# Kernel optimization log

Hardware: AMD Instinct MI355X
Metric: run time of the kernel (lower is better)

Reference implementation:

```python
import jax, jax.numpy as jnp
import numpy as np

NG, ND, CIN = 100000, 50000, 128
H, D = 8, 32
HID = H * D
E = 200000
SCALE = 1.0 / np.sqrt(D)


def _segment_softmax(logits, seg, num):
    # logits: [E, H]; softmax over edges sharing the same destination node
    m = jax.ops.segment_max(logits, seg, num_segments=num)
    m = jnp.where(jnp.isfinite(m), m, 0.0)  # guard empty segments
    e = jnp.exp(logits - m[seg])
    s = jax.ops.segment_sum(e, seg, num_segments=num)
    return e / (s[seg] + 1e-16)


def _kqv(x, Wk, bk, Wq, bq, Wv, bv):
    n = x.shape[0]
    return ((x @ Wk + bk).reshape(n, H, D),
            (x @ Wq + bq).reshape(n, H, D),
            (x @ Wv + bv).reshape(n, H, D))


def _message(k_src, v_src, q_dst, src, dst, a_rel, m_rel, p_rel, n_dst):
    # per-edge-type relation transform of gathered K/V, softmax over dst, scatter-add
    k_e = jnp.einsum('ehd,hdf->ehf', k_src[src], a_rel)          # [E,H,D]
    v_e = jnp.einsum('ehd,hdf->ehf', v_src[src], m_rel)          # [E,H,D]
    logits = jnp.einsum('ehf,ehf->eh', q_dst[dst], k_e) * p_rel * SCALE
    alpha = _segment_softmax(logits, dst, n_dst)                 # [E,H]
    return jax.ops.segment_sum(alpha[..., None] * v_e, dst, num_segments=n_dst)


def _forward(x_gene, x_disease, Win_g, bin_g, Wk_g, bk_g, Wq_g, bq_g, Wv_g, bv_g,
             Wa_g, ba_g, skip_g, Win_d, bin_d, Wk_d, bk_d, Wq_d, bq_d, Wv_d, bv_d,
             Wa_d, ba_d, skip_d, a_g2d, m_g2d, p_g2d, a_d2g, m_d2g, p_d2g,
             a_g2g, m_g2g, p_g2g, prelu_w,
             g2d_src, g2d_dst, d2g_src, d2g_dst, g2g_src, g2g_dst):
    # per-type input projection (Encoder.lin_dict)
    xg = x_gene @ Win_g + bin_g      # [NG, HID]
    xd = x_disease @ Win_d + bin_d   # [ND, HID]
    ng, nd = xg.shape[0], xd.shape[0]
    kg, qg, vg = _kqv(xg, Wk_g, bk_g, Wq_g, bq_g, Wv_g, bv_g)
    kd, qd, vd = _kqv(xd, Wk_d, bk_d, Wq_d, bq_d, Wv_d, bv_d)
    # HGTConv: message passing per edge type, summed per destination type
    out_d = _message(kg, vg, qd, g2d_src, g2d_dst, a_g2d, m_g2d, p_g2d, nd)
    out_g = (_message(kd, vd, qg, d2g_src, d2g_dst, a_d2g, m_d2g, p_d2g, ng)
             + _message(kg, vg, qg, g2g_src, g2g_dst, a_g2g, m_g2g, p_g2g, ng))

    def finish(out, x_proj, Wa, ba, skip):
        h = jax.nn.gelu(out.reshape(-1, HID), approximate=False) @ Wa + ba
        beta = jax.nn.sigmoid(skip)
        h = beta * h + (1.0 - beta) * x_proj          # HGT skip connection
        return jnp.where(h > 0, h, prelu_w * h)       # PReLU; Dropout=identity (eval)

    return (finish(out_g, xg, Wa_g, ba_g, skip_g),
            finish(out_d, xd, Wa_d, ba_d, skip_d))


def setup_inputs():
    key = jax.random.key(0)
    ki = iter(jax.random.split(key, 64))
    def nrm(shape, s):
        return (jax.random.normal(next(ki), shape) * s).astype(jnp.float32)
    inp = {}
    inp['x_gene'] = jax.random.normal(next(ki), (NG, CIN), jnp.float32)
    inp['x_disease'] = jax.random.normal(next(ki), (ND, CIN), jnp.float32)
    for t in ('g', 'd'):
        inp[f'Win_{t}'] = nrm((CIN, HID), 0.09)
        inp[f'bin_{t}'] = jnp.zeros((HID,), jnp.float32)
        for p in ('k', 'q', 'v'):
            inp[f'W{p}_{t}'] = nrm((HID, HID), 0.06)
            inp[f'b{p}_{t}'] = jnp.zeros((HID,), jnp.float32)
        inp[f'Wa_{t}'] = nrm((HID, HID), 0.06)
        inp[f'ba_{t}'] = jnp.zeros((HID,), jnp.float32)
        inp[f'skip_{t}'] = jnp.ones((1,), jnp.float32)
    for r in ('g2d', 'd2g', 'g2g'):
        inp[f'a_{r}'] = nrm((H, D, D), 0.18)
        inp[f'm_{r}'] = nrm((H, D, D), 0.18)
        inp[f'p_{r}'] = jnp.ones((H,), jnp.float32)
    inp['prelu_w'] = jnp.full((HID,), 0.25, jnp.float32)
    sizes = {'g2d': (NG, ND), 'd2g': (ND, NG), 'g2g': (NG, NG)}
    for r, (ns_, nd_) in sizes.items():
        inp[f'{r}_src'] = jax.random.randint(next(ki), (E,), 0, ns_, jnp.int32)
        inp[f'{r}_dst'] = jax.random.randint(next(ki), (E,), 0, nd_, jnp.int32)
    return inp


def reference(x_gene, x_disease, Win_g, bin_g, Wk_g, bk_g, Wq_g, bq_g, Wv_g, bv_g,
              Wa_g, ba_g, skip_g, Win_d, bin_d, Wk_d, bk_d, Wq_d, bq_d, Wv_d, bv_d,
              Wa_d, ba_d, skip_d, a_g2d, m_g2d, p_g2d, a_d2g, m_d2g, p_d2g,
              a_g2g, m_g2g, p_g2g, prelu_w,
              g2d_src, g2d_dst, d2g_src, d2g_dst, g2g_src, g2g_dst):
    return _forward(x_gene, x_disease, Win_g, bin_g, Wk_g, bk_g, Wq_g, bq_g, Wv_g, bv_g,
                    Wa_g, ba_g, skip_g, Win_d, bin_d, Wk_d, bk_d, Wq_d, bq_d, Wv_d, bv_d,
                    Wa_d, ba_d, skip_d, a_g2d, m_g2d, p_g2d, a_d2g, m_d2g, p_d2g,
                    a_g2g, m_g2g, p_g2g, prelu_w,
                    g2d_src, g2d_dst, d2g_src, d2g_dst, g2g_src, g2g_dst)
```

## Files before the change

kernel.cpp:

```cpp
#include <hip/hip_runtime.h>
#include <hip/hip_bf16.h>
#include <math.h>

typedef unsigned short u16;
typedef __attribute__((ext_vector_type(4))) float f32x4;
typedef __attribute__((ext_vector_type(8))) short s16x8;

__device__ __forceinline__ float b2f(u16 u){
  union { unsigned u; float f; } v; v.u = ((unsigned)u) << 16; return v.f;
}
__device__ __forceinline__ u16 f2b(float f){
  union { float f; unsigned u; } v; v.f = f;
  unsigned r = v.u + 0x7fffu + ((v.u >> 16) & 1u);
  return (u16)(r >> 16);
}

__device__ __forceinline__ void gload_lds(const u16* g, u16* l){
  __builtin_amdgcn_global_load_lds(
      (const __attribute__((address_space(1))) unsigned*)g,
      (__attribute__((address_space(3))) unsigned*)l, 16, 0, 0);
}

__global__ void zero_k(int* __restrict__ p, int n){
  int i = blockIdx.x*256 + threadIdx.x;
  if(i < n) p[i] = 0;
}

struct T6 { const float* W[6]; u16* O[6]; int K[6]; };
__global__ void transpose6(T6 a){
  int r = blockIdx.y;
  int idx = blockIdx.x*256 + threadIdx.x;
  int K = a.K[r];
  if(idx < K*256){ int k = idx >> 8, n = idx & 255; a.O[r][n*K + k] = f2b(a.W[r][idx]); }
}

struct F6 { const float* Wk[6]; const float* A[6]; u16* O[6]; };
__global__ void foldw6(F6 fa){
  int r = blockIdx.y;
  int idx = blockIdx.x*256 + threadIdx.x;
  int n = idx >> 8, k = idx & 255;
  int h = n >> 5, f = n & 31;
  const float* Wk = fa.Wk[r]; const float* A = fa.A[r];
  float s = 0.f;
  #pragma unroll 8
  for(int d = 0; d < 32; d++)
    s += Wk[k*256 + h*32 + d] * A[h*1024 + d*32 + f];
  fa.O[r][n*256 + k] = f2b(s);
}

struct Fb6 { const float* bk[6]; const float* A[6]; float* O[6]; };
__global__ void foldb6(Fb6 fa){
  int r = blockIdx.x;
  int n = threadIdx.x;
  int h = n >> 5, f = n & 31;
  float s = 0.f;
  for(int d = 0; d < 32; d++)
    s += fa.bk[r][h*32 + d] * fa.A[r][h*1024 + d*32 + f];
  fa.O[r][n] = s;
}

struct CSR3 {
  const int* src[3]; const int* dst[3]; int n[3];
  int* cnt[3]; int* rs[3]; int* cur[3]; int* col[3]; int* tot[3];
};
__global__ void count3(CSR3 c, int E){
  int r = blockIdx.y;
  int e = blockIdx.x*256 + threadIdx.x;
  if(e < E) atomicAdd(&c.cnt[r][c.dst[r][e]], 1);
}
__global__ void alloc3(CSR3 c){
  int r = blockIdx.y;
  int i = blockIdx.x*256 + threadIdx.x;
  if(i < c.n[r]) c.rs[r][i] = atomicAdd(c.tot[r], c.cnt[r][i]);
}
__global__ void fill3(CSR3 c, int E){
  int r = blockIdx.y;
  int e = blockIdx.x*256 + threadIdx.x;
  if(e < E){
    int d = c.dst[r][e];
    int p = c.rs[r][d] + atomicAdd(&c.cur[r][d], 1);
    c.col[r][p] = c.src[r][e];
  }
}

template<int AF, int EPI>
__global__ __launch_bounds__(256) void gemm128(
    const void* __restrict__ Ap, const u16* __restrict__ BT,
    const float* __restrict__ bias, void* __restrict__ Cout,
    int M, int K, int lda, int ldc,
    const u16* __restrict__ X, const float* __restrict__ skip,
    const float* __restrict__ prelu)
{
  constexpr int BM = (EPI == 2) ? 64 : 128;
  constexpr int BN = (EPI == 2) ? 256 : 128;
  __shared__ u16 As[BM*32];
  __shared__ u16 Bs[BN*32];
  const int t = threadIdx.x;
  const int m0 = blockIdx.x * BM;
  const int n0 = blockIdx.y * BN;
  const int w = t >> 6, lane = t & 63;
  const int wm = (EPI==2) ? 0 : ((w >> 1) << 6);
  const int wn = (EPI==2) ? (w << 6) : ((w & 1) << 6);
  const int lr = lane & 15, lq = lane >> 4;
  const int jr = lane >> 2;
  const int sp = lane & 3;
  f32x4 acc[4][4];
  #pragma unroll
  for(int i=0;i<4;i++)
    #pragma unroll
    for(int j=0;j<4;j++) acc[i][j] = (f32x4){0.f,0.f,0.f,0.f};

  for(int k0 = 0; k0 < K; k0 += 32){
    if(AF){
      const float* Af = (const float*)Ap;
      constexpr int NS = BM*4;
      #pragma unroll
      for(int j = 0; j < NS/256; j++){
        int s = t + j*256;
        int rr = s >> 2, p2 = s & 3;
        int sl = p2 ^ (rr & 3);
        int gm = m0 + rr; if(gm > M-1) gm = M-1;
        const float* g = Af + (size_t)gm*lda + k0 + sl*8;
        float4 f0 = *(const float4*)g;
        float4 f1 = *(const float4*)(g + 4);
        s16x8 v;
        v[0]=(short)f2b(f0.x); v[1]=(short)f2b(f0.y); v[2]=(short)f2b(f0.z); v[3]=(short)f2b(f0.w);
        v[4]=(short)f2b(f1.x); v[5]=(short)f2b(f1.y); v[6]=(short)f2b(f1.z); v[7]=(short)f2b(f1.w);
        *(s16x8*)&As[rr*32 + p2*8] = v;
      }
    } else {
      const u16* Ab = (const u16*)Ap;
      constexpr int RA = BM/4;
      #pragma unroll
      for(int i = 0; i < RA/16; i++){
        int rr = w*RA + i*16 + jr;
        int sl = sp ^ (rr & 3);
        int gm = m0 + rr; if(gm > M-1) gm = M-1;
        gload_lds(Ab + (size_t)gm*lda + k0 + sl*8, &As[(w*RA + i*16)*32]);
      }
    }
    {
      constexpr int RB = BN/4;
      #pragma unroll
      for(int i = 0; i < RB/16; i++){
        int rr = w*RB + i*16 + jr;
        int sl = sp ^ (rr & 3);
        gload_lds(BT + (size_t)(n0 + rr)*K + k0 + sl*8, &Bs[(w*RB + i*16)*32]);
      }
    }
    __syncthreads();
    s16x8 a[4], b[4];
    #pragma unroll
    for(int mt=0; mt<4; mt++)
      a[mt] = *(const s16x8*)&As[(wm + mt*16 + lr)*32 + ((lq ^ (lr&3)) << 3)];
    #pragma unroll
    for(int nt=0; nt<4; nt++)
      b[nt] = *(const s16x8*)&Bs[(wn + nt*16 + lr)*32 + ((lq ^ (lr&3)) << 3)];
    #pragma unroll
    for(int mt=0; mt<4; mt++)
      #pragma unroll
      for(int nt=0; nt<4; nt++)
        acc[mt][nt] = __builtin_amdgcn_mfma_f32_16x16x32_bf16(a[mt], b[nt], acc[mt][nt], 0, 0, 0);
    __syncthreads();
  }

  float beta = 0.f;
  if(EPI == 2) beta = 1.f/(1.f + __expf(-skip[0]));
  #pragma unroll
  for(int nt=0; nt<4; nt++){
    const int col = n0 + wn + nt*16 + lr;
    const float bcol = bias[col];
    float pw = 0.f;
    if(EPI == 2) pw = prelu[col];
    #pragma unroll
    for(int mt=0; mt<4; mt++){
      #pragma unroll
      for(int i=0;i<4;i++){
        int row = m0 + wm + mt*16 + lq*4 + i;
        if(row < M){
          float v = acc[mt][nt][i] + bcol;
          if(EPI == 0) ((u16*)Cout)[(size_t)row*ldc + col] = f2b(v);
          else if(EPI == 1) ((float*)Cout)[(size_t)row*ldc + col] = v;
          else {
            float xv = b2f(X[(size_t)row*256 + col]);
            v = beta*v + (1.f - beta)*xv;
            v = v > 0.f ? v : pw*v;
            ((float*)Cout)[(size_t)row*ldc + col] = v;
          }
        }
      }
    }
  }
}

template<int NREL>
__global__ __launch_bounds__(256) void message_gelu_k(
    const u16* __restrict__ KV1, const float* __restrict__ p1,
    const int* __restrict__ rs1, const int* __restrict__ cnt1, const int* __restrict__ col1,
    const u16* __restrict__ KV2, const float* __restrict__ p2,
    const int* __restrict__ rs2, const int* __restrict__ cnt2, const int* __restrict__ col2,
    float* __restrict__ Qio, int n_dst)
{
  int node = (blockIdx.x << 2) + (threadIdx.x >> 6);
  if(node >= n_dst) return;
  int lane = threadIdx.x & 63;
  float4 qv = *(const float4*)(Qio + (size_t)node*256 + (lane << 2));
  float q0=qv.x, q1=qv.y, q2=qv.z, q3=qv.w;
  float o0=0.f, o1=0.f, o2=0.f, o3=0.f;
  #pragma unroll
  for(int rel = 0; rel < NREL; rel++){
    const u16* KV = rel ? KV2 : KV1;
    const float* pr = rel ? p2 : p1;
    const int* rs = rel ? rs2 : rs1;
    const int* cn = rel ? cnt2 : cnt1;
    const int* cl = rel ? col2 : col1;
    float ps = pr[lane >> 3] * 0.17677669529663687f;
    float a0=0.f,a1=0.f,a2=0.f,a3=0.f,ss=0.f,mx=-1e30f;
    int r0 = rs[node], deg = cn[node];
    int i = 0;
    for(; i + 2 <= deg; i += 2){
      const u16* e0 = KV + (size_t)cl[r0+i]  *512 + (lane<<2);
      const u16* e1 = KV + (size_t)cl[r0+i+1]*512 + (lane<<2);
      ushort4 ka = *(const ushort4*)e0;
      ushort4 va = *(const ushort4*)(e0 + 256);
      ushort4 kb = *(const ushort4*)e1;
      ushort4 vb = *(const ushort4*)(e1 + 256);
      float da = q0*b2f(ka.x) + q1*b2f(ka.y) + q2*b2f(ka.z) + q3*b2f(ka.w);
      float db = q0*b2f(kb.x) + q1*b2f(kb.y) + q2*b2f(kb.z) + q3*b2f(kb.w);
      da += __shfl_xor(da, 1); da += __shfl_xor(da, 2); da += __shfl_xor(da, 4);
      db += __shfl_xor(db, 1); db += __shfl_xor(db, 2); db += __shfl_xor(db, 4);
      float la = da * ps, lb = db * ps;
      float nm = fmaxf(mx, fmaxf(la, lb));
      float c  = __expf(mx - nm);
      float wa = __expf(la - nm);
      float wb = __expf(lb - nm);
      mx = nm;
      ss = ss*c + wa + wb;
      a0 = a0*c + wa*b2f(va.x) + wb*b2f(vb.x);
      a1 = a1*c + wa*b2f(va.y) + wb*b2f(vb.y);
      a2 = a2*c + wa*b2f(va.z) + wb*b2f(vb.z);
      a3 = a3*c + wa*b2f(va.w) + wb*b2f(vb.w);
    }
    if(i < deg){
      const u16* e0 = KV + (size_t)cl[r0+i]*512 + (lane<<2);
      ushort4 ka = *(const ushort4*)e0;
      ushort4 va = *(const ushort4*)(e0 + 256);
      float da = q0*b2f(ka.x) + q1*b2f(ka.y) + q2*b2f(ka.z) + q3*b2f(ka.w);
      da += __shfl_xor(da, 1); da += __shfl_xor(da, 2); da += __shfl_xor(da, 4);
      float la = da * ps;
      float nm = fmaxf(mx, la);
      float c  = __expf(mx - nm);
      float wa = __expf(la - nm);
      mx = nm;
      ss = ss*c + wa;
      a0 = a0*c + wa*b2f(va.x);
      a1 = a1*c + wa*b2f(va.y);
      a2 = a2*c + wa*b2f(va.z);
      a3 = a3*c + wa*b2f(va.w);
    }
    float inv = 1.f/(ss + 1e-16f);
    o0 += a0*inv; o1 += a1*inv; o2 += a2*inv; o3 += a3*inv;
  }
  const float c = 0.70710678118654752f;
  float g0 = 0.5f*o0*(1.f + erff(o0*c));
  float g1 = 0.5f*o1*(1.f + erff(o1*c));
  float g2 = 0.5f*o2*(1.f + erff(o2*c));
  float g3 = 0.5f*o3*(1.f + erff(o3*c));
  ushort4 ov;
  ov.x = f2b(g0); ov.y = f2b(g1); ov.z = f2b(g2); ov.w = f2b(g3);
  *(ushort4*)((u16*)Qio + (size_t)node*512 + (lane << 2)) = ov;
}

extern "C" void kernel_launch(void* const* d_in, const int* in_sizes, int n_in,
                              void* d_out, int out_size, void* d_ws, size_t ws_size,
                              hipStream_t stream)
{
  (void)n_in; (void)out_size; (void)ws_size;
  #define IN_F32(i) ((const float*)d_in[i])
  #define IN_I32(i) ((const int*)d_in[i])
  const int NG = in_sizes[0] / 128;
  const int ND = in_sizes[1] / 128;
  const int E  = in_sizes[34];

  char* p = (char*)d_ws;
  auto carve = [&](size_t bytes) -> void* {
    void* q = (void*)p; p += (bytes + 255) & ~(size_t)255; return q;
  };
  u16* XG   = (u16*)carve((size_t)NG*256*2);
  u16* XD   = (u16*)carve((size_t)ND*256*2);
  u16* KVG  = (u16*)carve((size_t)NG*512*2);
  u16* KVD  = (u16*)carve((size_t)ND*512*2);
  u16* WTinG = (u16*)carve(256*128*2);
  u16* WTinD = (u16*)carve(256*128*2);
  u16* WTqG  = (u16*)carve(256*256*2);
  u16* WTqD  = (u16*)carve(256*256*2);
  u16* WTaG  = (u16*)carve(256*256*2);
  u16* WTaD  = (u16*)carve(256*256*2);
  u16* KVW[3]; for(int i=0;i<3;i++) KVW[i] = (u16*)carve(512*256*2);
  float* FBV[3]; for(int i=0;i<3;i++) FBV[i] = (float*)carve(512*4);
  const int zn = 2*(ND + 2*NG) + 8;
  int* zone = (int*)carve((size_t)zn*4);
  int* cnt0 = zone;
  int* cnt1 = cnt0 + ND;
  int* cnt2 = cnt1 + NG;
  int* cur0 = cnt2 + NG;
  int* cur1 = cur0 + ND;
  int* cur2 = cur1 + NG;
  int* tot  = cur2 + NG;
  int* rs0 = (int*)carve((size_t)ND*4);
  int* rs1 = (int*)carve((size_t)NG*4);
  int* rs2 = (int*)carve((size_t)NG*4);
  int* col0 = (int*)carve((size_t)E*4);
  int* col1 = (int*)carve((size_t)E*4);
  int* col2 = (int*)carve((size_t)E*4);

  float* QGio = (float*)d_out;
  float* QDio = (float*)d_out + (size_t)NG*256;

  {
    T6 a;
    const int wi[6] = {2,13,6,17,10,21};
    u16* wo[6] = {WTinG, WTinD, WTqG, WTqD, WTaG, WTaD};
    const int kk[6] = {128,128,256,256,256,256};
    for(int i=0;i<6;i++){ a.W[i]=IN_F32(wi[i]); a.O[i]=wo[i]; a.K[i]=kk[i]; }
    transpose6<<<dim3(256,6), 256, 0, stream>>>(a);
  }
  {
    F6 a; Fb6 b;
    const int wk[6] = {4,8,15,19,4,8};
    const int bk[6] = {5,9,16,20,5,9};
    const int am[6] = {24,25,27,28,30,31};
    for(int i=0;i<6;i++){
      a.Wk[i]=IN_F32(wk[i]); a.A[i]=IN_F32(am[i]);
      a.O[i] = KVW[i>>1] + (size_t)(i & 1)*256*256;
      b.bk[i]=IN_F32(bk[i]); b.A[i]=IN_F32(am[i]);
      b.O[i] = FBV[i>>1] + (i & 1)*256;
    }
    foldw6<<<dim3(256,6), 256, 0, stream>>>(a);
    foldb6<<<6, 256, 0, stream>>>(b);
  }
  CSR3 c;
  c.src[0]=IN_I32(34); c.dst[0]=IN_I32(35); c.n[0]=ND;
  c.src[1]=IN_I32(36); c.dst[1]=IN_I32(37); c.n[1]=NG;
  c.src[2]=IN_I32(38); c.dst[2]=IN_I32(39); c.n[2]=NG;
  c.cnt[0]=cnt0; c.cnt[1]=cnt1; c.cnt[2]=cnt2;
  c.cur[0]=cur0; c.cur[1]=cur1; c.cur[2]=cur2;
  c.rs[0]=rs0; c.rs[1]=rs1; c.rs[2]=rs2;
  c.col[0]=col0; c.col[1]=col1; c.col[2]=col2;
  c.tot[0]=tot; c.tot[1]=tot+1; c.tot[2]=tot+2;
  const int eb = (E + 255) / 256;
  const int nb = (NG + 255) / 256;
  zero_k<<<(zn + 255) / 256, 256, 0, stream>>>(zone, zn);
  count3<<<dim3(eb,3), 256, 0, stream>>>(c, E);
  alloc3<<<dim3(nb,3), 256, 0, stream>>>(c);
  fill3<<<dim3(eb,3), 256, 0, stream>>>(c, E);

  dim3 gG2((NG + 127)/128, 2), gD2((ND + 127)/128, 2);
  dim3 gG4((NG + 127)/128, 4), gD4((ND + 127)/128, 4);
  gemm128<1,0><<<gG2, 256, 0, stream>>>(d_in[0], WTinG, IN_F32(3),  XG, NG, 128, 128, 256, nullptr, nullptr, nullptr);
  gemm128<1,0><<<gD2, 256, 0, stream>>>(d_in[1], WTinD, IN_F32(14), XD, ND, 128, 128, 256, nullptr, nullptr, nullptr);

  gemm128<0,1><<<gD2, 256, 0, stream>>>(XD, WTqD,   IN_F32(18), QDio, ND, 256, 256, 256, nullptr, nullptr, nullptr);
  gemm128<0,0><<<gG4, 256, 0, stream>>>(XG, KVW[0], FBV[0],     KVG,  NG, 256, 256, 512, nullptr, nullptr, nullptr);
  message_gelu_k<1><<<(ND + 3) / 4, 256, 0, stream>>>(
      KVG, IN_F32(26), rs0, cnt0, col0,
      nullptr, nullptr, nullptr, nullptr, nullptr,
      QDio, ND);

  gemm128<0,1><<<gG2, 256, 0, stream>>>(XG, WTqG,   IN_F32(7), QGio, NG, 256, 256, 256, nullptr, nullptr, nullptr);
  gemm128<0,0><<<gD4, 256, 0, stream>>>(XD, KVW[1], FBV[1],    KVD,  ND, 256, 256, 512, nullptr, nullptr, nullptr);
  gemm128<0,0><<<gG4, 256, 0, stream>>>(XG, KVW[2], FBV[2],    KVG,  NG, 256, 256, 512, nullptr, nullptr, nullptr);
  message_gelu_k<2><<<(NG + 3) / 4, 256, 0, stream>>>(
      KVD, IN_F32(29), rs1, cnt1, col1,
      KVG, IN_F32(32), rs2, cnt2, col2,
      QGio, NG);

  gemm128<0,2><<<dim3((NG + 63)/64, 1), 256, 0, stream>>>(
      (const u16*)QGio, WTaG, IN_F32(11), QGio, NG, 256, 512, 256, XG, IN_F32(12), IN_F32(33));
  gemm128<0,2><<<dim3((ND + 63)/64, 1), 256, 0, stream>>>(
      (const u16*)QDio, WTaD, IN_F32(22), QDio, ND, 256, 512, 256, XD, IN_F32(23), IN_F32(33));
  #undef IN_F32
  #undef IN_I32
}
```

Before: 1.133 ms.

## Batch independent GEMMs into grouped launches with XCD-aware block swizzle

Replaces the separate per-matrix GEMM launches with grouped kernels that handle up to four GEMMs in one grid, picking the problem from a per-block offset table. Block IDs are remapped so consecutive tiles land on the same XCD, aiming for better L2 reuse. The bf16 output epilogue is staged through LDS so global stores become row-contiguous 16-byte writes. The final epilogue GEMMs for both node types are merged into one launch. This cuts launch count and tail effects but adds per-block dispatch logic and extra barriers in the epilogue.

After: 1.043 ms. 8.0% less time.

```diff
diff --git a/kernel.cpp b/kernel.cpp
--- a/kernel.cpp
+++ b/kernel.cpp
@@ -19,6 +19,12 @@
   __builtin_amdgcn_global_load_lds(
       (const __attribute__((address_space(1))) unsigned*)g,
       (__attribute__((address_space(3))) unsigned*)l, 16, 0, 0);
+}
+
+__device__ __forceinline__ int chunk_swz(int bid, int nwg){
+  int q = nwg >> 3, r = nwg & 7;
+  int xcd = bid & 7, off = bid >> 3;
+  return (xcd < r ? xcd*(q+1) : r*(q+1) + (xcd-r)*q) + off;
 }
 
 __global__ void zero_k(int* __restrict__ p, int n){
@@ -83,24 +89,31 @@
   }
 }
 
-template<int AF, int EPI>
-__global__ __launch_bounds__(256) void gemm128(
-    const void* __restrict__ Ap, const u16* __restrict__ BT,
-    const float* __restrict__ bias, void* __restrict__ Cout,
-    int M, int K, int lda, int ldc,
-    const u16* __restrict__ X, const float* __restrict__ skip,
-    const float* __restrict__ prelu)
-{
-  constexpr int BM = (EPI == 2) ? 64 : 128;
-  constexpr int BN = (EPI == 2) ? 256 : 128;
-  __shared__ u16 As[BM*32];
-  __shared__ u16 Bs[BN*32];
+struct GMD {
+  const void* A; const u16* BT; const float* bias; void* C;
+  int M, K, lda, ldc, lgy, base, epi;
+};
+struct GM4 { GMD g[4]; int n, nblk; };
+
+template<int AF>
+__global__ __launch_bounds__(256) void gemm_multi(GM4 P){
+  __shared__ u16 sh[128*64];
+  u16* As = sh;
+  u16* Bs = sh + 128*32;
   const int t = threadIdx.x;
-  const int m0 = blockIdx.x * BM;
-  const int n0 = blockIdx.y * BN;
+  const int l = chunk_swz(blockIdx.x, P.nblk);
+  int g = 0;
+  #pragma unroll
+  for(int i = 1; i < 4; i++) if(i < P.n && l >= P.g[i].base) g = i;
+  const GMD d = P.g[g];
+  const int local = l - d.base;
+  const int x = local >> d.lgy;
+  const int y = local & ((1 << d.lgy) - 1);
+  const int m0 = x << 7, n0 = y << 7;
+  const int M = d.M, K = d.K, lda = d.lda, ldc = d.ldc;
   const int w = t >> 6, lane = t & 63;
-  const int wm = (EPI==2) ? 0 : ((w >> 1) << 6);
-  const int wn = (EPI==2) ? (w << 6) : ((w & 1) << 6);
+  const int wm = (w >> 1) << 6;
+  const int wn = (w & 1) << 6;
   const int lr = lane & 15, lq = lane >> 4;
   const int jr = lane >> 2;
   const int sp = lane & 3;
@@ -112,41 +125,36 @@
 
   for(int k0 = 0; k0 < K; k0 += 32){
     if(AF){
-      const float* Af = (const float*)Ap;
-      constexpr int NS = BM*4;
+      const float* Af = (const float*)d.A;
       #pragma unroll
-      for(int j = 0; j < NS/256; j++){
+      for(int j = 0; j < 2; j++){
         int s = t + j*256;
         int rr = s >> 2, p2 = s & 3;
         int sl = p2 ^ (rr & 3);
         int gm = m0 + rr; if(gm > M-1) gm = M-1;
-        const float* g = Af + (size_t)gm*lda + k0 + sl*8;
-        float4 f0 = *(const float4*)g;
-        float4 f1 = *(const float4*)(g + 4);
+        const float* gp = Af + (size_t)gm*lda + k0 + sl*8;
+        float4 f0 = *(const float4*)gp;
+        float4 f1 = *(const float4*)(gp + 4);
         s16x8 v;
         v[0]=(short)f2b(f0.x); v[1]=(short)f2b(f0.y); v[2]=(short)f2b(f0.z); v[3]=(short)f2b(f0.w);
         v[4]=(short)f2b(f1.x); v[5]=(short)f2b(f1.y); v[6]=(short)f2b(f1.z); v[7]=(short)f2b(f1.w);
         *(s16x8*)&As[rr*32 + p2*8] = v;
       }
     } else {
-      const u16* Ab = (const u16*)Ap;
-      constexpr int RA = BM/4;
+      const u16* Ab = (const u16*)d.A;
       #pragma unroll
-      for(int i = 0; i < RA/16; i++){
-        int rr = w*RA + i*16 + jr;
+      for(int i = 0; i < 2; i++){
+        int rr = w*32 + i*16 + jr;
         int sl = sp ^ (rr & 3);
         int gm = m0 + rr; if(gm > M-1) gm = M-1;
-        gload_lds(Ab + (size_t)gm*lda + k0 + sl*8, &As[(w*RA + i*16)*32]);
+        gload_lds(Ab + (size_t)gm*lda + k0 + sl*8, &As[(w*32 + i*16)*32]);
       }
     }
-    {
-      constexpr int RB = BN/4;
-      #pragma unroll
-      for(int i = 0; i < RB/16; i++){
-        int rr = w*RB + i*16 + jr;
-        int sl = sp ^ (rr & 3);
-        gload_lds(BT + (size_t)(n0 + rr)*K + k0 + sl*8, &Bs[(w*RB + i*16)*32]);
-      }
+    #pragma unroll
+    for(int i = 0; i < 2; i++){
+      int rr = w*32 + i*16 + jr;
+      int sl = sp ^ (rr & 3);
+      gload_lds(d.BT + (size_t)(n0 + rr)*K + k0 + sl*8, &Bs[(w*32 + i*16)*32]);
     }
     __syncthreads();
     s16x8 a[4], b[4];
@@ -164,29 +172,125 @@
     __syncthreads();
   }
 
-  float beta = 0.f;
-  if(EPI == 2) beta = 1.f/(1.f + __expf(-skip[0]));
+  if(d.epi == 1){
+    float* C = (float*)d.C;
+    #pragma unroll
+    for(int nt=0; nt<4; nt++){
+      const int col = n0 + wn + nt*16 + lr;
+      const float bc = d.bias[col];
+      #pragma unroll
+      for(int mt=0; mt<4; mt++)
+        #pragma unroll
+        for(int i=0;i<4;i++){
+          int row = m0 + wm + mt*16 + lq*4 + i;
+          if(row < M) C[(size_t)row*ldc + col] = acc[mt][nt][i] + bc;
+        }
+    }
+  } else {
+    u16* C = (u16*)d.C;
+    #pragma unroll
+    for(int p = 0; p < 2; p++){
+      if((w & 1) == p){
+        #pragma unroll
+        for(int nt=0; nt<4; nt++){
+          const int cp = nt*16 + lr;
+          const float bc = d.bias[n0 + p*64 + cp];
+          #pragma unroll
+          for(int mt=0; mt<4; mt++)
+            #pragma unroll
+            for(int i=0;i<4;i++){
+              int row = wm + mt*16 + lq*4 + i;
+              int so = (cp >> 3) ^ (row & 7);
+              sh[row*64 + so*8 + (cp & 7)] = f2b(acc[mt][nt][i] + bc);
+            }
+        }
+      }
+      __syncthreads();
+      {
+        int row = t >> 1, hh = t & 1;
+        if(m0 + row < M){
+          u16* dst = C + (size_t)(m0 + row)*ldc + n0 + p*64 + hh*32;
+          #pragma unroll
+          for(int j=0;j<4;j++){
+            int so = (hh*4 + j) ^ (row & 7);
+            *(s16x8*)(dst + j*8) = *(const s16x8*)&sh[row*64 + so*8];
+          }
+        }
+      }
+      __syncthreads();
+    }
+  }
+}
+
+struct GE { const u16* A; const u16* BT; const float* bias; float* C;
+            const u16* X; const float* skip; const float* prelu; int M, base; };
+struct GE2 { GE g[2]; int nblk; };
+
+__global__ __launch_bounds__(256) void gemm_epi2(GE2 P){
+  __shared__ u16 As[64*32];
+  __shared__ u16 Bs[256*32];
+  const int t = threadIdx.x;
+  const int l = chunk_swz(blockIdx.x, P.nblk);
+  const int g = (l >= P.g[1].base) ? 1 : 0;
+  const GE d = P.g[g];
+  const int m0 = (l - d.base) << 6;
+  const int M = d.M;
+  const int w = t >> 6, lane = t & 63;
+  const int wn = w << 6;
+  const int lr = lane & 15, lq = lane >> 4;
+  const int jr = lane >> 2, sp = lane & 3;
+  f32x4 acc[4][4];
+  #pragma unroll
+  for(int i=0;i<4;i++)
+    #pragma unroll
+    for(int j=0;j<4;j++) acc[i][j] = (f32x4){0.f,0.f,0.f,0.f};
+
+  for(int k0 = 0; k0 < 256; k0 += 32){
+    {
+      int rr = w*16 + jr;
+      int sl = sp ^ (rr & 3);
+      int gm = m0 + rr; if(gm > M-1) gm = M-1;
+      gload_lds(d.A + (size_t)gm*512 + k0 + sl*8, &As[(w*16)*32]);
+    }
+    #pragma unroll
+    for(int i = 0; i < 4; i++){
+      int rr = w*64 + i*16 + jr;
+      int sl = sp ^ (rr & 3);
+      gload_lds(d.BT + (size_t)rr*256 + k0 + sl*8, &Bs[(w*64 + i*16)*32]);
+    }
+    __syncthreads();
+    s16x8 a[4], b[4];
+    #pragma unroll
+    for(int mt=0; mt<4; mt++)
+      a[mt] = *(const s16x8*)&As[(mt*16 + lr)*32 + ((lq ^ (lr&3)) << 3)];
+    #pragma unroll
+    for(int nt=0; nt<4; nt++)
+      b[nt] = *(const s16x8*)&Bs[(wn + nt*16 + lr)*32 + ((lq ^ (lr&3)) << 3)];
+    #pragma unroll
+    for(int mt=0; mt<4; mt++)
+      #pragma unroll
+      for(int nt=0; nt<4; nt++)
+        acc[mt][nt] = __builtin_amdgcn_mfma_f32_16x16x32_bf16(a[mt], b[nt], acc[mt][nt], 0, 0, 0);
+    __syncthreads();
+  }
+
+  const float beta = 1.f/(1.f + __expf(-d.skip[0]));
   #pragma unroll
   for(int nt=0; nt<4; nt++){
-    const int col = n0 + wn + nt*16 + lr;
-    const float bcol = bias[col];
-    float pw = 0.f;
-    if(EPI == 2) pw = prelu[col];
+    const int col = wn + nt*16 + lr;
+    const float bc = d.bias[col];
+    const float pw = d.prelu[col];
     #pragma unroll
     for(int mt=0; mt<4; mt++){
       #pragma unroll
       for(int i=0;i<4;i++){
-        int row = m0 + wm + mt*16 + lq*4 + i;
+        int row = m0 + mt*16 + lq*4 + i;
         if(row < M){
-          float v = acc[mt][nt][i] + bcol;
-          if(EPI == 0) ((u16*)Cout)[(size_t)row*ldc + col] = f2b(v);
-          else if(EPI == 1) ((float*)Cout)[(size_t)row*ldc + col] = v;
-          else {
-            float xv = b2f(X[(size_t)row*256 + col]);
-            v = beta*v + (1.f - beta)*xv;
-            v = v > 0.f ? v : pw*v;
-            ((float*)Cout)[(size_t)row*ldc + col] = v;
-          }
+          float v = acc[mt][nt][i] + bc;
+          float xv = b2f(d.X[(size_t)row*256 + col]);
+          v = beta*v + (1.f - beta)*xv;
+          v = v > 0.f ? v : pw*v;
+          d.C[(size_t)row*256 + col] = v;
         }
       }
     }
@@ -355,30 +459,71 @@
   alloc3<<<dim3(nb,3), 256, 0, stream>>>(c);
   fill3<<<dim3(eb,3), 256, 0, stream>>>(c, E);
 
-  dim3 gG2((NG + 127)/128, 2), gD2((ND + 127)/128, 2);
-  dim3 gG4((NG + 127)/128, 4), gD4((ND + 127)/128, 4);
-  gemm128<1,0><<<gG2, 256, 0, stream>>>(d_in[0], WTinG, IN_F32(3),  XG, NG, 128, 128, 256, nullptr, nullptr, nullptr);
-  gemm128<1,0><<<gD2, 256, 0, stream>>>(d_in[1], WTinD, IN_F32(14), XD, ND, 128, 128, 256, nullptr, nullptr, nullptr);
-
-  gemm128<0,1><<<gD2, 256, 0, stream>>>(XD, WTqD,   IN_F32(18), QDio, ND, 256, 256, 256, nullptr, nullptr, nullptr);
-  gemm128<0,0><<<gG4, 256, 0, stream>>>(XG, KVW[0], FBV[0],     KVG,  NG, 256, 256, 512, nullptr, nullptr, nullptr);
+  const int xg = (NG + 127)/128, xd = (ND + 127)/128;
+
+  {
+    GM4 pj{};
+    pj.g[0].A = d_in[0]; pj.g[0].BT = WTinG; pj.g[0].bias = IN_F32(3);  pj.g[0].C = XG;
+    pj.g[0].M = NG; pj.g[0].K = 128; pj.g[0].lda = 128; pj.g[0].ldc = 256;
+    pj.g[0].lgy = 1; pj.g[0].base = 0; pj.g[0].epi = 0;
+    pj.g[1].A = d_in[1]; pj.g[1].BT = WTinD; pj.g[1].bias = IN_F32(14); pj.g[1].C = XD;
+    pj.g[1].M = ND; pj.g[1].K = 128; pj.g[1].lda = 128; pj.g[1].ldc = 256;
+    pj.g[1].lgy = 1; pj.g[1].base = xg*2; pj.g[1].epi = 0;
+    pj.n = 2; pj.nblk = xg*2 + xd*2;
+    gemm_multi<1><<<pj.nblk, 256, 0, stream>>>(pj);
+  }
+
+  {
+    GM4 md{};
+    md.g[0].A = XD; md.g[0].BT = WTqD;   md.g[0].bias = IN_F32(18); md.g[0].C = QDio;
+    md.g[0].M = ND; md.g[0].K = 256; md.g[0].lda = 256; md.g[0].ldc = 256;
+    md.g[0].lgy = 1; md.g[0].base = 0; md.g[0].epi = 1;
+    int b1 = xd*2;
+    md.g[1].A = XG; md.g[1].BT = KVW[0]; md.g[1].bias = FBV[0]; md.g[1].C = KVG;
+    md.g[1].M = NG; md.g[1].K = 256; md.g[1].lda = 256; md.g[1].ldc = 512;
+    md.g[1].lgy = 2; md.g[1].base = b1; md.g[1].epi = 0;
+    int b2 = b1 + xg*4;
+    md.g[2].A = XG; md.g[2].BT = WTqG;   md.g[2].bias = IN_F32(7); md.g[2].C = QGio;
+    md.g[2].M = NG; md.g[2].K = 256; md.g[2].lda = 256; md.g[2].ldc = 256;
+    md.g[2].lgy = 1; md.g[2].base = b2; md.g[2].epi = 1;
+    int b3 = b2 + xg*2;
+    md.g[3].A = XD; md.g[3].BT = KVW[1]; md.g[3].bias = FBV[1]; md.g[3].C = KVD;
+    md.g[3].M = ND; md.g[3].K = 256; md.g[3].lda = 256; md.g[3].ldc = 512;
+    md.g[3].lgy = 2; md.g[3].base = b3; md.g[3].epi = 0;
+    md.n = 4; md.nblk = b3 + xd*4;
+    gemm_multi<0><<<md.nblk, 256, 0, stream>>>(md);
+  }
+
   message_gelu_k<1><<<(ND + 3) / 4, 256, 0, stream>>>(
       KVG, IN_F32(26), rs0, cnt0, col0,
       nullptr, nullptr, nullptr, nullptr, nullptr,
       QDio, ND);
 
-  gemm128<0,1><<<gG2, 256, 0, stream>>>(XG, WTqG,   IN_F32(7), QGio, NG, 256, 256, 256, nullptr, nullptr, nullptr);
-  gemm128<0,0><<<gD4, 256, 0, stream>>>(XD, KVW[1], FBV[1],    KVD,  ND, 256, 256, 512, nullptr, nullptr, nullptr);
-  gemm128<0,0><<<gG4, 256, 0, stream>>>(XG, KVW[2], FBV[2],    KVG,  NG, 256, 256, 512, nullptr, nullptr, nullptr);
+  {
+    GM4 k2{};
+    k2.g[0].A = XG; k2.g[0].BT = KVW[2]; k2.g[0].bias = FBV[2]; k2.g[0].C = KVG;
+    k2.g[0].M = NG; k2.g[0].K = 256; k2.g[0].lda = 256; k2.g[0].ldc = 512;
+    k2.g[0].lgy = 2; k2.g[0].base = 0; k2.g[0].epi = 0;
+    k2.n = 1; k2.nblk = xg*4;
+    gemm_multi<0><<<k2.nblk, 256, 0, stream>>>(k2);
+  }
+
   message_gelu_k<2><<<(NG + 3) / 4, 256, 0, stream>>>(
       KVD, IN_F32(29), rs1, cnt1, col1,
       KVG, IN_F32(32), rs2, cnt2, col2,
       QGio, NG);
 
-  gemm128<0,2><<<dim3((NG + 63)/64, 1), 256, 0, stream>>>(
-      (const u16*)QGio, WTaG, IN_F32(11), QGio, NG, 256, 512, 256, XG, IN_F32(12), IN_F32(33));
-  gemm128<0,2><<<dim3((ND + 63)/64, 1), 256, 0, stream>>>(
-      (const u16*)QDio, WTaD, IN_F32(22), QDio, ND, 256, 512, 256, XD, IN_F32(23), IN_F32(33));
+  {
+    GE2 ep{};
+    ep.g[0].A = (const u16*)QGio; ep.g[0].BT = WTaG; ep.g[0].bias = IN_F32(11);
+    ep.g[0].C = QGio; ep.g[0].X = XG; ep.g[0].skip = IN_F32(12); ep.g[0].prelu = IN_F32(33);
+    ep.g[0].M = NG; ep.g[0].base = 0;
+    ep.g[1].A = (const u16*)QDio; ep.g[1].BT = WTaD; ep.g[1].bias = IN_F32(22);
+    ep.g[1].C = QDio; ep.g[1].X = XD; ep.g[1].skip = IN_F32(23); ep.g[1].prelu = IN_F32(33);
+    ep.g[1].M = ND; ep.g[1].base = (NG + 63)/64;
+    ep.nblk = (NG + 63)/64 + (ND + 63)/64;
+    gemm_epi2<<<ep.nblk, 256, 0, stream>>>(ep);
+  }
   #undef IN_F32
   #undef IN_I32
 }
```
